# Kernel optimization log

Measured on AMD Instinct MI355X. Metric: run time of the kernel, lower is better.

## Reference

```python
import jax, jax.numpy as jnp
import numpy as np

IN_FEATURES = 4096
OUT_FEATURES = 4096
GROUPS = 1
QB = 2 ** (8 - 1) - 1  # 127, int8 absmax quant


def setup_inputs() -> dict:
    key = jax.random.key(0)
    k_x, k_w = jax.random.split(key)
    x = jax.random.normal(k_x, (8192, IN_FEATURES), dtype=jnp.float32)
    # kaiming_uniform_(a=sqrt(5)) -> uniform(-1/sqrt(in), 1/sqrt(in))
    bound = 1.0 / np.sqrt(IN_FEATURES)
    weight = jax.random.uniform(
        k_w, (OUT_FEATURES, IN_FEATURES), dtype=jnp.float32,
        minval=-bound, maxval=bound)
    return {"input": x, "weight": weight}


def reference(input, weight):
    # --- ternarize weight per group ---
    w = weight.reshape(GROUPS, -1)                       # [G, out*in/G]
    w = w - jnp.mean(w, axis=1, keepdims=True)
    w = jnp.sign(w)
    # beta: per-group scale (note denominator uses full element count, as in source)
    beta = jnp.sum(jnp.abs(w), axis=1, keepdims=True) / (w.shape[0] * w.shape[1])
    w = (w * beta).reshape(OUT_FEATURES, IN_FEATURES)    # [out, in]

    # --- absmax int8 quantize activations (quantized values used, not dequant) ---
    scale = QB / jnp.max(jnp.abs(input))
    quant = jnp.round(scale * input)                     # [tokens, in]

    # --- linear + rescale ---
    out = quant @ w.T                                    # [tokens, out]
    out = out / beta.reshape(-1, 1)                      # groups=1: scalar divide
    return out
```

## Files before the change

### kernel.cpp

```cpp
#include <hip/hip_runtime.h>
#include <hip/hip_bf16.h>

typedef __attribute__((ext_vector_type(4))) int int4v;

#define TOKENS 8192
#define IN_F   4096
#define OUT_F  4096


__global__ __launch_bounds__(256) void k_wsum(const float4* __restrict__ w,
                                              double* __restrict__ partials,
                                              unsigned* __restrict__ maxbits) {
  if (blockIdx.x == 0 && threadIdx.x == 0) *maxbits = 0u;
  __shared__ double sm[256];
  double s = 0.0;
  const float4* p = w + (size_t)blockIdx.x * 4096;
  for (int i = threadIdx.x; i < 4096; i += 256) {
    float4 v = p[i];
    s += (double)v.x + (double)v.y + (double)v.z + (double)v.w;
  }
  sm[threadIdx.x] = s;
  __syncthreads();
  for (int off = 128; off > 0; off >>= 1) {
    if (threadIdx.x < off) sm[threadIdx.x] += sm[threadIdx.x + off];
    __syncthreads();
  }
  if (threadIdx.x == 0) partials[blockIdx.x] = sm[0];
}

__global__ __launch_bounds__(256) void k_xmax(const float4* __restrict__ x,
                                              unsigned* __restrict__ maxbits) {
  float m = 0.f;
  const size_t n = (size_t)TOKENS * IN_F / 4;
  for (size_t i = (size_t)blockIdx.x * 256 + threadIdx.x; i < n;
       i += (size_t)gridDim.x * 256) {
    float4 v = x[i];
    m = fmaxf(m, fmaxf(fmaxf(fabsf(v.x), fabsf(v.y)),
                       fmaxf(fabsf(v.z), fabsf(v.w))));
  }
  __shared__ float sm[256];
  sm[threadIdx.x] = m;
  __syncthreads();
  for (int off = 128; off > 0; off >>= 1) {
    if (threadIdx.x < off) sm[threadIdx.x] = fmaxf(sm[threadIdx.x], sm[threadIdx.x + off]);
    __syncthreads();
  }
  if (threadIdx.x == 0) atomicMax(maxbits, __float_as_uint(sm[0]));
}

__global__ __launch_bounds__(256) void k_finalize(double* __restrict__ hdr,
                                                  const double* __restrict__ partials,
                                                  const unsigned* __restrict__ maxbits) {
  __shared__ double sm[256];
  double s = partials[threadIdx.x] + partials[threadIdx.x + 256] +
             partials[threadIdx.x + 512] + partials[threadIdx.x + 768];
  sm[threadIdx.x] = s;
  __syncthreads();
  for (int off = 128; off > 0; off >>= 1) {
    if (threadIdx.x < off) sm[threadIdx.x] += sm[threadIdx.x + off];
    __syncthreads();
  }
  if (threadIdx.x == 0) {
    hdr[0] = sm[0] / (double)((size_t)OUT_F * IN_F);
    hdr[1] = 127.0 / (double)__uint_as_float(*maxbits);
  }
}

#define QB_BLK ((TOKENS * IN_F / 4) / 256)
#define TB_BLK ((OUT_F * IN_F / 4) / 256)
__global__ __launch_bounds__(256) void k_quant_tern(const float4* __restrict__ x,
                                                    const float4* __restrict__ w,
                                                    int* __restrict__ q,
                                                    int* __restrict__ sgn,
                                                    const double* __restrict__ hdr) {
  if (blockIdx.x < QB_BLK) {
    const double s = hdr[1];
    size_t i = (size_t)blockIdx.x * 256 + threadIdx.x;
    float4 v = x[i];
    int a = (int)rint(s * (double)v.x);
    int b = (int)rint(s * (double)v.y);
    int c = (int)rint(s * (double)v.z);
    int d = (int)rint(s * (double)v.w);
    q[i] = (a & 255) | ((b & 255) << 8) | ((c & 255) << 16) | ((d & 255) << 24);
  } else {
    const double m = hdr[0];
    size_t i = (size_t)(blockIdx.x - QB_BLK) * 256 + threadIdx.x;
    float4 v = w[i];
    int a = ((double)v.x > m) - ((double)v.x < m);
    int b = ((double)v.y > m) - ((double)v.y < m);
    int c = ((double)v.z > m) - ((double)v.z < m);
    int d = ((double)v.w > m) - ((double)v.w < m);
    sgn[i] = (a & 255) | ((b & 255) << 8) | ((c & 255) << 16) | ((d & 255) << 24);
  }
}

__device__ __forceinline__ void stage2(const signed char* __restrict__ gsrc,
                                       size_t grow0, int ktile,
                                       signed char* ldsbase, int tid, int wid) {
#pragma unroll
  for (int i = 0; i < 2; ++i) {
    const int slot = i * 512 + tid;
    const int r = slot >> 2;
    const int sir = slot & 3;
    const signed char* g = gsrc + (grow0 + (size_t)r) * IN_F +
                           (size_t)ktile * 64 + ((sir ^ ((r >> 1) & 3)) << 4);
    __builtin_amdgcn_global_load_lds(
        (const __attribute__((address_space(1))) void*)g,
        (__attribute__((address_space(3))) void*)(ldsbase + (i * 512 + wid * 64) * 16),
        16, 0, 0);
  }
}

__global__ __launch_bounds__(512, 2) void k_gemm(const signed char* __restrict__ q,
                                                 const signed char* __restrict__ s,
                                                 float* __restrict__ out) {
  __shared__ signed char sA[4][256 * 64];
  __shared__ signed char sB[4][256 * 64];
  const int tid  = threadIdx.x;
  const int lane = tid & 63;
  const int wid  = tid >> 6;
  const int wm   = wid >> 2;
  const int wn   = wid & 3;
  const int l15  = lane & 15, l4 = lane >> 4;

  const int swz = (blockIdx.x & 7) * 64 + (blockIdx.x >> 3);
  const int bm = swz >> 4;
  const int bn = swz & 15;
  const size_t row0 = (size_t)bm * 256;
  const size_t col0 = (size_t)bn * 256;

  const int lane_off = l15 * 64 + ((l4 ^ ((l15 >> 1) & 3)) << 4);

  int4v acc[8][4];
#pragma unroll
  for (int i = 0; i < 8; ++i)
#pragma unroll
    for (int j = 0; j < 4; ++j) acc[i][j] = int4v{0, 0, 0, 0};

#pragma unroll
  for (int t = 0; t < 3; ++t) {
    stage2(q, row0, t, sA[t], tid, wid);
    stage2(s, col0, t, sB[t], tid, wid);
  }
  asm volatile("s_waitcnt vmcnt(8)" ::: "memory");
  __builtin_amdgcn_sched_barrier(0);
  __builtin_amdgcn_s_barrier();
  __builtin_amdgcn_sched_barrier(0);

  for (int kt = 0; kt < 64; ++kt) {
    const int c = kt & 3;
    const int pf   = (kt + 3) & 63;
    const int pbuf = (kt + 3) & 3;
    const signed char* bufA = sA[c];
    const signed char* bufB = sB[c];

    int4v a[8], b0, b1;
#pragma unroll
    for (int m = 0; m < 8; ++m)
      a[m] = *(const int4v*)(bufA + (wm * 128 + m * 16) * 64 + lane_off);
    b0 = *(const int4v*)(bufB + (wn * 64 + 0) * 64 + lane_off);
    b1 = *(const int4v*)(bufB + (wn * 64 + 16) * 64 + lane_off);
    stage2(q, row0, pf, sA[pbuf], tid, wid);
    __builtin_amdgcn_sched_barrier(0);
    __builtin_amdgcn_s_barrier();
    asm volatile("s_waitcnt lgkmcnt(0)" ::: "memory");
    __builtin_amdgcn_sched_barrier(0);
    __builtin_amdgcn_s_setprio(1);
#pragma unroll
    for (int m = 0; m < 8; ++m) {
      acc[m][0] = __builtin_amdgcn_mfma_i32_16x16x64_i8(a[m], b0, acc[m][0], 0, 0, 0);
      acc[m][1] = __builtin_amdgcn_mfma_i32_16x16x64_i8(a[m], b1, acc[m][1], 0, 0, 0);
    }
    __builtin_amdgcn_s_setprio(0);
    __builtin_amdgcn_sched_barrier(0);
    __builtin_amdgcn_s_barrier();

    int4v b2 = *(const int4v*)(bufB + (wn * 64 + 32) * 64 + lane_off);
    int4v b3 = *(const int4v*)(bufB + (wn * 64 + 48) * 64 + lane_off);
    stage2(s, col0, pf, sB[pbuf], tid, wid);
    __builtin_amdgcn_sched_barrier(0);
    __builtin_amdgcn_s_barrier();
    asm volatile("s_waitcnt lgkmcnt(0)" ::: "memory");
    __builtin_amdgcn_sched_barrier(0);
    __builtin_amdgcn_s_setprio(1);
#pragma unroll
    for (int m = 0; m < 8; ++m) {
      acc[m][2] = __builtin_amdgcn_mfma_i32_16x16x64_i8(a[m], b2, acc[m][2], 0, 0, 0);
      acc[m][3] = __builtin_amdgcn_mfma_i32_16x16x64_i8(a[m], b3, acc[m][3], 0, 0, 0);
    }
    __builtin_amdgcn_s_setprio(0);
    asm volatile("s_waitcnt vmcnt(8)" ::: "memory");
    __builtin_amdgcn_sched_barrier(0);
    __builtin_amdgcn_s_barrier();
    __builtin_amdgcn_sched_barrier(0);
  }

#pragma unroll
  for (int m = 0; m < 8; ++m)
#pragma unroll
    for (int n = 0; n < 4; ++n)
#pragma unroll
      for (int r = 0; r < 4; ++r) {
        const size_t rg = row0 + wm * 128 + m * 16 + l4 * 4 + r;
        const size_t cg = col0 + wn * 64 + n * 16 + l15;
        out[rg * OUT_F + cg] = (float)acc[m][n][r];
      }
}

extern "C" void kernel_launch(void* const* d_in, const int* in_sizes, int n_in,
                              void* d_out, int out_size, void* d_ws, size_t ws_size,
                              hipStream_t stream) {
  const float* x = (const float*)d_in[0];
  const float* w = (const float*)d_in[1];
  float* out = (float*)d_out;

  char* ws = (char*)d_ws;
  double*   hdr      = (double*)ws;
  unsigned* maxbits  = (unsigned*)(ws + 16);
  double*   partials = (double*)(ws + 1024);
  signed char* qbuf  = (signed char*)(ws + 16384);
  signed char* sbuf  = (signed char*)(ws + 16384 + (size_t)TOKENS * IN_F);

  k_wsum<<<1024, 256, 0, stream>>>((const float4*)w, partials, maxbits);
  k_xmax<<<2048, 256, 0, stream>>>((const float4*)x, maxbits);
  k_finalize<<<1, 256, 0, stream>>>(hdr, partials, maxbits);
  k_quant_tern<<<QB_BLK + TB_BLK, 256, 0, stream>>>((const float4*)x, (const float4*)w,
                                                    (int*)qbuf, (int*)sbuf, hdr);
  k_gemm<<<(TOKENS / 256) * (OUT_F / 256), 512, 0, stream>>>(qbuf, sbuf, out);
}
```

Measured before the change: 236.1 us.

## Shrink GEMM tile to 256x128 with double buffering and fuse reduction kernels

```diff
diff --git a/kernel.cpp b/kernel.cpp
--- a/kernel.cpp
+++ b/kernel.cpp
@@ -8,61 +8,67 @@
 #define OUT_F  4096
 
 
-__global__ __launch_bounds__(256) void k_wsum(const float4* __restrict__ w,
-                                              double* __restrict__ partials,
-                                              unsigned* __restrict__ maxbits) {
-  if (blockIdx.x == 0 && threadIdx.x == 0) *maxbits = 0u;
+__global__ __launch_bounds__(256) void k_pre(const float4* __restrict__ w,
+                                             const float4* __restrict__ x,
+                                             double* __restrict__ partials,
+                                             float* __restrict__ xpart) {
+  if (blockIdx.x < 1024) {
+    __shared__ double sm[256];
+    double s = 0.0;
+    const float4* p = w + (size_t)blockIdx.x * 4096;
+    for (int i = threadIdx.x; i < 4096; i += 256) {
+      float4 v = p[i];
+      s += (double)v.x + (double)v.y + (double)v.z + (double)v.w;
+    }
+    sm[threadIdx.x] = s;
+    __syncthreads();
+    for (int off = 128; off > 0; off >>= 1) {
+      if (threadIdx.x < off) sm[threadIdx.x] += sm[threadIdx.x + off];
+      __syncthreads();
+    }
+    if (threadIdx.x == 0) partials[blockIdx.x] = sm[0];
+  } else {
+    const int b = blockIdx.x - 1024;
+    float m = 0.f;
+    const size_t n = (size_t)TOKENS * IN_F / 4;
+    for (size_t i = (size_t)b * 256 + threadIdx.x; i < n; i += (size_t)1024 * 256) {
+      float4 v = x[i];
+      m = fmaxf(m, fmaxf(fmaxf(fabsf(v.x), fabsf(v.y)),
+                         fmaxf(fabsf(v.z), fabsf(v.w))));
+    }
+    __shared__ float smf[256];
+    smf[threadIdx.x] = m;
+    __syncthreads();
+    for (int off = 128; off > 0; off >>= 1) {
+      if (threadIdx.x < off) smf[threadIdx.x] = fmaxf(smf[threadIdx.x], smf[threadIdx.x + off]);
+      __syncthreads();
+    }
+    if (threadIdx.x == 0) xpart[b] = smf[0];
+  }
+}
+
+__global__ __launch_bounds__(256) void k_finalize(double* __restrict__ hdr,
+                                                  const double* __restrict__ partials,
+                                                  const float* __restrict__ xpart) {
   __shared__ double sm[256];
-  double s = 0.0;
-  const float4* p = w + (size_t)blockIdx.x * 4096;
-  for (int i = threadIdx.x; i < 4096; i += 256) {
-    float4 v = p[i];
-    s += (double)v.x + (double)v.y + (double)v.z + (double)v.w;
-  }
+  __shared__ float smf[256];
+  double s = partials[threadIdx.x] + partials[threadIdx.x + 256] +
+             partials[threadIdx.x + 512] + partials[threadIdx.x + 768];
+  float m = fmaxf(fmaxf(xpart[threadIdx.x], xpart[threadIdx.x + 256]),
+                  fmaxf(xpart[threadIdx.x + 512], xpart[threadIdx.x + 768]));
   sm[threadIdx.x] = s;
+  smf[threadIdx.x] = m;
   __syncthreads();
   for (int off = 128; off > 0; off >>= 1) {
-    if (threadIdx.x < off) sm[threadIdx.x] += sm[threadIdx.x + off];
-    __syncthreads();
-  }
-  if (threadIdx.x == 0) partials[blockIdx.x] = sm[0];
-}
-
-__global__ __launch_bounds__(256) void k_xmax(const float4* __restrict__ x,
-                                              unsigned* __restrict__ maxbits) {
-  float m = 0.f;
-  const size_t n = (size_t)TOKENS * IN_F / 4;
-  for (size_t i = (size_t)blockIdx.x * 256 + threadIdx.x; i < n;
-       i += (size_t)gridDim.x * 256) {
-    float4 v = x[i];
-    m = fmaxf(m, fmaxf(fmaxf(fabsf(v.x), fabsf(v.y)),
-                       fmaxf(fabsf(v.z), fabsf(v.w))));
-  }
-  __shared__ float sm[256];
-  sm[threadIdx.x] = m;
-  __syncthreads();
-  for (int off = 128; off > 0; off >>= 1) {
-    if (threadIdx.x < off) sm[threadIdx.x] = fmaxf(sm[threadIdx.x], sm[threadIdx.x + off]);
-    __syncthreads();
-  }
-  if (threadIdx.x == 0) atomicMax(maxbits, __float_as_uint(sm[0]));
-}
-
-__global__ __launch_bounds__(256) void k_finalize(double* __restrict__ hdr,
-                                                  const double* __restrict__ partials,
-                                                  const unsigned* __restrict__ maxbits) {
-  __shared__ double sm[256];
-  double s = partials[threadIdx.x] + partials[threadIdx.x + 256] +
-             partials[threadIdx.x + 512] + partials[threadIdx.x + 768];
-  sm[threadIdx.x] = s;
-  __syncthreads();
-  for (int off = 128; off > 0; off >>= 1) {
-    if (threadIdx.x < off) sm[threadIdx.x] += sm[threadIdx.x + off];
+    if (threadIdx.x < off) {
+      sm[threadIdx.x] += sm[threadIdx.x + off];
+      smf[threadIdx.x] = fmaxf(smf[threadIdx.x], smf[threadIdx.x + off]);
+    }
     __syncthreads();
   }
   if (threadIdx.x == 0) {
     hdr[0] = sm[0] / (double)((size_t)OUT_F * IN_F);
-    hdr[1] = 127.0 / (double)__uint_as_float(*maxbits);
+    hdr[1] = 127.0 / (double)smf[0];
   }
 }
 
@@ -94,7 +100,7 @@
   }
 }
 
-__device__ __forceinline__ void stage2(const signed char* __restrict__ gsrc,
+__device__ __forceinline__ void stageA(const signed char* __restrict__ gsrc,
                                        size_t grow0, int ktile,
                                        signed char* ldsbase, int tid, int wid) {
 #pragma unroll
@@ -111,99 +117,95 @@
   }
 }
 
-__global__ __launch_bounds__(512, 2) void k_gemm(const signed char* __restrict__ q,
+__device__ __forceinline__ void stageB(const signed char* __restrict__ gsrc,
+                                       size_t grow0, int ktile,
+                                       signed char* ldsbase, int tid, int wid) {
+  const int r = tid >> 2;
+  const int sir = tid & 3;
+  const signed char* g = gsrc + (grow0 + (size_t)r) * IN_F +
+                         (size_t)ktile * 64 + ((sir ^ ((r >> 1) & 3)) << 4);
+  __builtin_amdgcn_global_load_lds(
+      (const __attribute__((address_space(1))) void*)g,
+      (__attribute__((address_space(3))) void*)(ldsbase + (wid * 64) * 16),
+      16, 0, 0);
+}
+
+__global__ __launch_bounds__(512, 4) void k_gemm(const signed char* __restrict__ q,
                                                  const signed char* __restrict__ s,
                                                  float* __restrict__ out) {
-  __shared__ signed char sA[4][256 * 64];
-  __shared__ signed char sB[4][256 * 64];
+  __shared__ signed char sA[2][256 * 64];
+  __shared__ signed char sB[2][128 * 64];
   const int tid  = threadIdx.x;
   const int lane = tid & 63;
   const int wid  = tid >> 6;
-  const int wm   = wid >> 2;
-  const int wn   = wid & 3;
+  const int wm   = wid >> 1;
+  const int wn   = wid & 1;
   const int l15  = lane & 15, l4 = lane >> 4;
 
-  const int swz = (blockIdx.x & 7) * 64 + (blockIdx.x >> 3);
-  const int bm = swz >> 4;
-  const int bn = swz & 15;
+  const int swz = (blockIdx.x & 7) * 128 + (blockIdx.x >> 3);
+  const int bm = swz >> 5;
+  const int bn = swz & 31;
   const size_t row0 = (size_t)bm * 256;
-  const size_t col0 = (size_t)bn * 256;
+  const size_t col0 = (size_t)bn * 128;
 
   const int lane_off = l15 * 64 + ((l4 ^ ((l15 >> 1) & 3)) << 4);
 
-  int4v acc[8][4];
-#pragma unroll
-  for (int i = 0; i < 8; ++i)
+  int4v acc[4][4];
+#pragma unroll
+  for (int i = 0; i < 4; ++i)
 #pragma unroll
     for (int j = 0; j < 4; ++j) acc[i][j] = int4v{0, 0, 0, 0};
 
-#pragma unroll
-  for (int t = 0; t < 3; ++t) {
-    stage2(q, row0, t, sA[t], tid, wid);
-    stage2(s, col0, t, sB[t], tid, wid);
-  }
-  asm volatile("s_waitcnt vmcnt(8)" ::: "memory");
+  stageA(q, row0, 0, sA[0], tid, wid);
+  stageB(s, col0, 0, sB[0], tid, wid);
+  asm volatile("s_waitcnt vmcnt(0)" ::: "memory");
   __builtin_amdgcn_sched_barrier(0);
   __builtin_amdgcn_s_barrier();
   __builtin_amdgcn_sched_barrier(0);
 
   for (int kt = 0; kt < 64; ++kt) {
-    const int c = kt & 3;
-    const int pf   = (kt + 3) & 63;
-    const int pbuf = (kt + 3) & 3;
+    const int c = kt & 1;
     const signed char* bufA = sA[c];
     const signed char* bufB = sB[c];
 
-    int4v a[8], b0, b1;
-#pragma unroll
-    for (int m = 0; m < 8; ++m)
-      a[m] = *(const int4v*)(bufA + (wm * 128 + m * 16) * 64 + lane_off);
-    b0 = *(const int4v*)(bufB + (wn * 64 + 0) * 64 + lane_off);
-    b1 = *(const int4v*)(bufB + (wn * 64 + 16) * 64 + lane_off);
-    stage2(q, row0, pf, sA[pbuf], tid, wid);
+    if (kt != 63) {
+      stageA(q, row0, kt + 1, sA[c ^ 1], tid, wid);
+      stageB(s, col0, kt + 1, sB[c ^ 1], tid, wid);
+    }
+    __builtin_amdgcn_sched_barrier(0);
+
+    int4v a[4], b[4];
+#pragma unroll
+    for (int f = 0; f < 4; ++f)
+      a[f] = *(const int4v*)(bufA + (wm * 64 + f * 16) * 64 + lane_off);
+#pragma unroll
+    for (int f = 0; f < 4; ++f)
+      b[f] = *(const int4v*)(bufB + (wn * 64 + f * 16) * 64 + lane_off);
+    asm volatile("s_waitcnt lgkmcnt(0)" ::: "memory");
+    __builtin_amdgcn_sched_barrier(0);
+    __builtin_amdgcn_s_setprio(1);
+#pragma unroll
+    for (int fm = 0; fm < 4; ++fm)
+#pragma unroll
+      for (int fn = 0; fn < 4; ++fn)
+        acc[fm][fn] = __builtin_amdgcn_mfma_i32_16x16x64_i8(a[fm], b[fn], acc[fm][fn], 0, 0, 0);
+    __builtin_amdgcn_s_setprio(0);
+    __builtin_amdgcn_sched_barrier(0);
+    asm volatile("s_waitcnt vmcnt(0)" ::: "memory");
     __builtin_amdgcn_sched_barrier(0);
     __builtin_amdgcn_s_barrier();
-    asm volatile("s_waitcnt lgkmcnt(0)" ::: "memory");
-    __builtin_amdgcn_sched_barrier(0);
-    __builtin_amdgcn_s_setprio(1);
-#pragma unroll
-    for (int m = 0; m < 8; ++m) {
-      acc[m][0] = __builtin_amdgcn_mfma_i32_16x16x64_i8(a[m], b0, acc[m][0], 0, 0, 0);
-      acc[m][1] = __builtin_amdgcn_mfma_i32_16x16x64_i8(a[m], b1, acc[m][1], 0, 0, 0);
-    }
-    __builtin_amdgcn_s_setprio(0);
-    __builtin_amdgcn_sched_barrier(0);
-    __builtin_amdgcn_s_barrier();
-
-    int4v b2 = *(const int4v*)(bufB + (wn * 64 + 32) * 64 + lane_off);
-    int4v b3 = *(const int4v*)(bufB + (wn * 64 + 48) * 64 + lane_off);
-    stage2(s, col0, pf, sB[pbuf], tid, wid);
-    __builtin_amdgcn_sched_barrier(0);
-    __builtin_amdgcn_s_barrier();
-    asm volatile("s_waitcnt lgkmcnt(0)" ::: "memory");
-    __builtin_amdgcn_sched_barrier(0);
-    __builtin_amdgcn_s_setprio(1);
-#pragma unroll
-    for (int m = 0; m < 8; ++m) {
-      acc[m][2] = __builtin_amdgcn_mfma_i32_16x16x64_i8(a[m], b2, acc[m][2], 0, 0, 0);
-      acc[m][3] = __builtin_amdgcn_mfma_i32_16x16x64_i8(a[m], b3, acc[m][3], 0, 0, 0);
-    }
-    __builtin_amdgcn_s_setprio(0);
-    asm volatile("s_waitcnt vmcnt(8)" ::: "memory");
-    __builtin_amdgcn_sched_barrier(0);
-    __builtin_amdgcn_s_barrier();
-    __builtin_amdgcn_sched_barrier(0);
-  }
-
-#pragma unroll
-  for (int m = 0; m < 8; ++m)
-#pragma unroll
-    for (int n = 0; n < 4; ++n)
+    __builtin_amdgcn_sched_barrier(0);
+  }
+
+#pragma unroll
+  for (int fm = 0; fm < 4; ++fm)
+#pragma unroll
+    for (int fn = 0; fn < 4; ++fn)
 #pragma unroll
       for (int r = 0; r < 4; ++r) {
-        const size_t rg = row0 + wm * 128 + m * 16 + l4 * 4 + r;
-        const size_t cg = col0 + wn * 64 + n * 16 + l15;
-        out[rg * OUT_F + cg] = (float)acc[m][n][r];
+        const size_t rg = row0 + wm * 64 + fm * 16 + l4 * 4 + r;
+        const size_t cg = col0 + wn * 64 + fn * 16 + l15;
+        out[rg * OUT_F + cg] = (float)acc[fm][fn][r];
       }
 }
 
@@ -216,15 +218,14 @@
 
   char* ws = (char*)d_ws;
   double*   hdr      = (double*)ws;
-  unsigned* maxbits  = (unsigned*)(ws + 16);
   double*   partials = (double*)(ws + 1024);
+  float*    xpart    = (float*)(ws + 9216);
   signed char* qbuf  = (signed char*)(ws + 16384);
   signed char* sbuf  = (signed char*)(ws + 16384 + (size_t)TOKENS * IN_F);
 
-  k_wsum<<<1024, 256, 0, stream>>>((const float4*)w, partials, maxbits);
-  k_xmax<<<2048, 256, 0, stream>>>((const float4*)x, maxbits);
-  k_finalize<<<1, 256, 0, stream>>>(hdr, partials, maxbits);
+  k_pre<<<2048, 256, 0, stream>>>((const float4*)w, (const float4*)x, partials, xpart);
+  k_finalize<<<1, 256, 0, stream>>>(hdr, partials, xpart);
   k_quant_tern<<<QB_BLK + TB_BLK, 256, 0, stream>>>((const float4*)x, (const float4*)w,
                                                     (int*)qbuf, (int*)sbuf, hdr);
-  k_gemm<<<(TOKENS / 256) * (OUT_F / 256), 512, 0, stream>>>(qbuf, sbuf, out);
-}
+  k_gemm<<<(TOKENS / 256) * (OUT_F / 128), 512, 0, stream>>>(qbuf, sbuf, out);
+}
```

Measured after the change: 231.1 us. -2.1%, faster.
